# Optimization experiments

Measured on AMD Instinct MI355X. Metric: run time of the kernel, lower is better.

The kernel has to match this reference:

```python
import jax, jax.numpy as jnp
import numpy as np

EPS = 1e-5

def group_points(feat, idx):
    # feat: [B, C, N1], idx: [B, N2, K] -> [B, C, N2, K]
    return jax.vmap(lambda f, i: f[:, i])(feat, idx)

def conv_bn_relu(x, W, gamma, beta):
    # 1x1 conv2d (no bias) + training-mode BatchNorm2d + ReLU
    y = jnp.einsum('oc,bcnk->bonk', W, x)
    mean = y.mean(axis=(0, 2, 3), keepdims=True)
    var = y.var(axis=(0, 2, 3), keepdims=True)  # biased, as BN uses for normalization
    y = (y - mean) * jax.lax.rsqrt(var + EPS)
    y = y * gamma[None, :, None, None] + beta[None, :, None, None]
    return jax.nn.relu(y)

def setup_inputs() -> dict:
    key = jax.random.key(0)
    ks = jax.random.split(key, 12)
    B, N1, N2, K, C1 = 16, 4096, 1024, 32, 64
    mlp = [C1 + 3, 64, 64, 128]  # use_xyz adds 3 channels
    inp = {
        'in_xyz': jax.random.normal(ks[0], (B, 3, N1), jnp.float32),
        'out_xyz': jax.random.normal(ks[1], (B, 3, N2), jnp.float32),
        'in_feature': jax.random.normal(ks[2], (B, C1, N1), jnp.float32),
        'nbr_index': jax.random.randint(ks[3], (B, N2, K), 0, N1, jnp.int32),
    }
    for li in range(3):
        cin, cout = mlp[li], mlp[li + 1]
        inp[f'W{li}'] = jax.random.normal(ks[4 + li], (cout, cin), jnp.float32) * (1.0 / np.sqrt(cin))
        inp[f'g{li}'] = jnp.ones((cout,), jnp.float32)
        inp[f'b{li}'] = jnp.zeros((cout,), jnp.float32)
    return inp

def reference(in_xyz, out_xyz, in_feature, nbr_index,
              W0, g0, b0, W1, g1, b1, W2, g2, b2):
    # gather neighbor features: [B, C1, N2, K]
    nbr_feature = group_points(in_feature, nbr_index)
    # gather neighbor xyz, recenter on query points: [B, 3, N2, K]
    nbr_xyz = group_points(in_xyz, nbr_index) - out_xyz[:, :, :, None]
    x = jnp.concatenate([nbr_feature, nbr_xyz], axis=1)  # [B, C1+3, N2, K]
    x = conv_bn_relu(x, W0, g0, b0)
    x = conv_bn_relu(x, W1, g1, b1)
    x = conv_bn_relu(x, W2, g2, b2)
    return jnp.max(x, axis=3)  # [B, C2, N2]
```

## Files before the change

### kernel.cpp

```cpp
#include <hip/hip_runtime.h>
#include <cstdint>

typedef unsigned short u16;
typedef unsigned int   u32;
typedef __attribute__((ext_vector_type(8))) short  short8;
typedef __attribute__((ext_vector_type(4))) float  floatx4;

#define NPTS 524288

__device__ __forceinline__ float b2f(u16 h) { return __uint_as_float(((u32)h) << 16); }
__device__ __forceinline__ u16 f2b(float f) {
  u32 u = __float_as_uint(f);
  return (u16)((u + 0x7FFFu + ((u >> 16) & 1u)) >> 16);
}
__device__ __forceinline__ u32 pk_bf16(float lo, float hi) {
  return (u32)f2b(lo) | ((u32)f2b(hi) << 16);
}
__device__ __forceinline__ short8 ld_frag8(const u16* p) {
  union { uint4 q; short8 s; } x;
  x.q = *(const uint4*)p;
  return x.s;
}
__device__ __forceinline__ void bar_lds() {
  asm volatile("s_waitcnt lgkmcnt(0)\n\ts_barrier" ::: "memory");
}

__global__ __launch_bounds__(256) void prep_all(const float* __restrict__ inf,
                                                const float* __restrict__ ixyz,
                                                const float* __restrict__ oxyz,
                                                const int* __restrict__ nbr,
                                                const float* __restrict__ W0,
                                                const float* __restrict__ W1,
                                                const float* __restrict__ W2,
                                                u16* __restrict__ featT,
                                                uint2* __restrict__ dxyz,
                                                u16* __restrict__ Wb,
                                                u32* __restrict__ cnt,
                                                float* __restrict__ accz) {
  __shared__ float tile[32 * 33];
  const int bk = blockIdx.x, t = threadIdx.x;
  if (bk < 4096) {
    int b = bk >> 8, rem = bk & 255, cc = rem >> 7, nc = rem & 127;
    #pragma unroll
    for (int i = 0; i < 4; ++i) {
      int flat = t + i * 256;
      int cl = flat >> 5, nl = flat & 31;
      tile[cl * 33 + nl] = inf[(size_t)((b * 64) + cc * 32 + cl) * 4096 + nc * 32 + nl];
    }
    __syncthreads();
    #pragma unroll
    for (int i = 0; i < 4; ++i) {
      int flat = t + i * 256;
      int nl = flat >> 5, cl = flat & 31;
      featT[(size_t)((b << 12) + nc * 32 + nl) * 64 + cc * 32 + cl] = f2b(tile[cl * 33 + nl]);
    }
  } else if (bk < 6144) {
    int g = (bk - 4096) * 256 + t;
    int b = g >> 15, r = g & 32767, n2 = r >> 5;
    int id = nbr[g];
    const float* ix = ixyz + (size_t)b * 12288;
    const float* ox = oxyz + (size_t)b * 3072;
    float dx = ix[id]        - ox[n2];
    float dy = ix[4096 + id] - ox[1024 + n2];
    float dzv = ix[8192 + id] - ox[2048 + n2];
    dxyz[g] = make_uint2(pk_bf16(dx, dy), pk_bf16(dzv, 0.f));
  } else {
    int s = (bk - 6144) * 256 + t;
    u16 v = 0;
    if (s < 6656)       { int o = s / 104, c = s % 104; if (c < 67) v = f2b(W0[o * 67 + c]); }
    else if (s < 11264) { int q = s - 6656;  int o = q / 72, c = q % 72; if (c < 64) v = f2b(W1[o * 64 + c]); }
    else                { int q = s - 11264; int o = q / 72, c = q % 72; if (c < 64) v = f2b(W2[o * 64 + c]); }
    Wb[s] = v;
    if (bk == 6144) {
      if (t < 4) cnt[t] = 0u;
      accz[t] = 0.f;
      accz[256 + t] = 0.f;
    }
  }
}

template<int KSTEPS, int OCH, bool GATHER, bool MAXOUT>
__global__ __launch_bounds__(256, 4) void gemm_layer(
    const u16* __restrict__ xsrc, const uint2* __restrict__ dxyz,
    const int* __restrict__ nbr,
    const u16* __restrict__ Wb, const float* __restrict__ ssin,
    u16* __restrict__ yout, u32* __restrict__ gm,
    float* __restrict__ partial) {
  constexpr int PITCH = KSTEPS * 32 + 8;
  __shared__ __align__(16) u16 xs[2][64 * PITCH];
  __shared__ float red[512];
  __shared__ float ss[GATHER ? 4 : 128];

  const int t = threadIdx.x, blk = blockIdx.x;
  const int lane = t & 63, wv = t >> 6, lr = lane & 15, quad = lane >> 4;
  const int m = t >> 2, s4 = t & 3;
  const int P0 = blk * 256;
  const int b = blk >> 7;
  const int rg = wv >> 1, cg = wv & 1;

  short8 wf[4][KSTEPS];
  #pragma unroll
  for (int nt = 0; nt < 4; ++nt) {
    const int orow = (MAXOUT ? cg * 64 : 0) + nt * 16 + lr;
    const u16* wr = Wb + orow * PITCH + quad * 8;
    #pragma unroll
    for (int ks = 0; ks < KSTEPS; ++ks)
      wf[nt][ks] = ld_frag8(wr + ks * 32);
  }

  if constexpr (!GATHER) {
    if (t < 128) ss[t] = ssin[t];
  }
  if constexpr (GATHER) {
    #pragma unroll
    for (int bu = 0; bu < 2; ++bu) {
      if (s4 == 1) {
        u16* xr = xs[bu] + m * PITCH;
        #pragma unroll
        for (int j = 0; j < 9; ++j) *(uint2*)(xr + 68 + j * 4) = make_uint2(0u, 0u);
      }
    }
  }
  if constexpr (!GATHER) __syncthreads();

  int idx4[4];
  if constexpr (GATHER) {
    #pragma unroll
    for (int sub = 0; sub < 4; ++sub) idx4[sub] = nbr[P0 + sub * 64 + m];
  }

  uint4 f0, f1;
  uint2 dz = make_uint2(0u, 0u);

  auto issue = [&](int sub) {
    const int P = P0 + sub * 64 + m;
    if constexpr (GATHER) {
      const int id = idx4[sub];
      const u16* row = xsrc + ((size_t)((b << 12) + id)) * 64;
      f0 = *(const uint4*)(row + s4 * 16);
      f1 = *(const uint4*)(row + s4 * 16 + 8);
      if (s4 == 0) dz = dxyz[P];
    } else {
      const u16* row = xsrc + ((size_t)P << 6);
      f0 = *(const uint4*)(row + s4 * 16);
      f1 = *(const uint4*)(row + s4 * 16 + 8);
    }
  };

  auto commit = [&](int bu) {
    u16* xrow = xs[bu] + m * PITCH + s4 * 16;
    if constexpr (GATHER) {
      *(uint4*)(xrow + 0) = f0;
      *(uint4*)(xrow + 8) = f1;
      if (s4 == 0) *(uint2*)(xs[bu] + m * PITCH + 64) = dz;
    } else {
      u32 w[8] = { f0.x, f0.y, f0.z, f0.w, f1.x, f1.y, f1.z, f1.w };
      u32 o[8];
      #pragma unroll
      for (int i = 0; i < 8; ++i) {
        const int c = s4 * 16 + i * 2;
        float lo = fmaxf(b2f((u16)(w[i] & 0xffffu)) * ss[c]     + ss[64 + c],     0.f);
        float hi = fmaxf(b2f((u16)(w[i] >> 16))     * ss[c + 1] + ss[64 + c + 1], 0.f);
        o[i] = pk_bf16(lo, hi);
      }
      *(uint4*)(xrow + 0) = make_uint4(o[0], o[1], o[2], o[3]);
      *(uint4*)(xrow + 8) = make_uint4(o[4], o[5], o[6], o[7]);
    }
  };

  issue(0); commit(0);
  issue(1);
  __syncthreads();

  float s1[4] = {0.f, 0.f, 0.f, 0.f}, s2[4] = {0.f, 0.f, 0.f, 0.f};
  u32* yo = (u32*)yout;

  for (int sub = 0; sub < 4; ++sub) {
    const int cur = sub & 1;
    if (sub < 3) commit(cur ^ 1);
    if (sub < 2) issue(sub + 2);

    if constexpr (!MAXOUT) {
      const u16* ap = xs[cur] + (wv * 16 + lr) * PITCH + quad * 8;
      floatx4 acc[4];
      #pragma unroll
      for (int nt = 0; nt < 4; ++nt) acc[nt] = (floatx4){0.f, 0.f, 0.f, 0.f};
      #pragma unroll
      for (int ks = 0; ks < KSTEPS; ++ks) {
        short8 av = ld_frag8(ap + ks * 32);
        #pragma unroll
        for (int nt = 0; nt < 4; ++nt)
          acc[nt] = __builtin_amdgcn_mfma_f32_16x16x32_bf16(av, wf[nt][ks], acc[nt], 0, 0, 0);
      }
      const int R0 = P0 + sub * 64 + wv * 16 + quad * 4;
      #pragma unroll
      for (int nt = 0; nt < 4; ++nt) {
        #pragma unroll
        for (int r = 0; r < 4; ++r) {
          float v = acc[nt][r];
          s1[nt] += v; s2[nt] += v * v;
          float vo = __shfl_xor(v, 1);
          if ((lr & 1) == 0)
            yo[(size_t)(R0 + r) * 32 + nt * 8 + (lr >> 1)] = pk_bf16(v, vo);
        }
      }
    } else {
      short8 av[2][KSTEPS];
      #pragma unroll
      for (int h = 0; h < 2; ++h)
        #pragma unroll
        for (int ks = 0; ks < KSTEPS; ++ks)
          av[h][ks] = ld_frag8(xs[cur] + (rg * 32 + h * 16 + lr) * PITCH + quad * 8 + ks * 32);
      floatx4 acc[2][4];
      #pragma unroll
      for (int h = 0; h < 2; ++h)
        #pragma unroll
        for (int nt = 0; nt < 4; ++nt) acc[h][nt] = (floatx4){0.f, 0.f, 0.f, 0.f};
      #pragma unroll
      for (int ks = 0; ks < KSTEPS; ++ks)
        #pragma unroll
        for (int nt = 0; nt < 4; ++nt)
          #pragma unroll
          for (int h = 0; h < 2; ++h)
            acc[h][nt] = __builtin_amdgcn_mfma_f32_16x16x32_bf16(av[h][ks], wf[nt][ks], acc[h][nt], 0, 0, 0);
      float mx[4], mn[4];
      #pragma unroll
      for (int nt = 0; nt < 4; ++nt) {
        mx[nt] = -INFINITY; mn[nt] = INFINITY;
        #pragma unroll
        for (int h = 0; h < 2; ++h)
          #pragma unroll
          for (int r = 0; r < 4; ++r) {
            float v = acc[h][nt][r];
            s1[nt] += v; s2[nt] += v * v;
            mx[nt] = fmaxf(mx[nt], v); mn[nt] = fminf(mn[nt], v);
          }
        mx[nt] = fmaxf(mx[nt], __shfl_xor(mx[nt], 16));
        mx[nt] = fmaxf(mx[nt], __shfl_xor(mx[nt], 32));
        mn[nt] = fminf(mn[nt], __shfl_xor(mn[nt], 16));
        mn[nt] = fminf(mn[nt], __shfl_xor(mn[nt], 32));
      }
      if (lane < 16) {
        const int grp = blk * 8 + sub * 2 + rg;
        #pragma unroll
        for (int nt = 0; nt < 4; ++nt)
          gm[(size_t)grp * 128 + cg * 64 + nt * 16 + lr] = pk_bf16(mx[nt], mn[nt]);
      }
    }
    if (sub < 3) bar_lds();
  }

  #pragma unroll
  for (int nt = 0; nt < 4; ++nt) {
    s1[nt] += __shfl_xor(s1[nt], 16); s1[nt] += __shfl_xor(s1[nt], 32);
    s2[nt] += __shfl_xor(s2[nt], 16); s2[nt] += __shfl_xor(s2[nt], 32);
  }
  if (lane < 16) {
    #pragma unroll
    for (int nt = 0; nt < 4; ++nt) {
      red[wv * 64 + nt * 16 + lr] = s1[nt];
      red[256 + wv * 64 + nt * 16 + lr] = s2[nt];
    }
  }
  __syncthreads();
  if constexpr (!MAXOUT) {
    if (t < 64) {
      partial[(size_t)blk * 128 + t] = red[t] + red[64 + t] + red[128 + t] + red[192 + t];
    } else if (t < 128) {
      int c = t - 64;
      partial[(size_t)blk * 128 + t] = red[256 + c] + red[320 + c] + red[384 + c] + red[448 + c];
    }
  } else {
    if (t < 128) {
      int half = t >> 6, i = t & 63;
      partial[(size_t)blk * 256 + t] = red[half * 64 + i] + red[(half + 2) * 64 + i];
    } else {
      int c = t - 128, half = c >> 6, i = c & 63;
      partial[(size_t)blk * 256 + t] = red[256 + half * 64 + i] + red[256 + (half + 2) * 64 + i];
    }
  }
}

__global__ __launch_bounds__(256) void bn_stats(const float* __restrict__ partial,
                                                float* __restrict__ accv,
                                                const float* __restrict__ gam,
                                                const float* __restrict__ bet,
                                                float* __restrict__ ssout,
                                                u32* __restrict__ counter, int och) {
  __shared__ float l[256];
  __shared__ u32 rank;
  const int cols = 2 * och, t = threadIdx.x;
  if (t < cols) {
    const size_t r0 = (size_t)blockIdx.x * 32;
    float s = 0.f;
    for (int r = 0; r < 32; ++r) s += partial[(r0 + r) * cols + t];
    atomicAdd(&accv[t], s);
  }
  __threadfence();
  __syncthreads();
  if (t == 0) rank = atomicAdd(counter, 1u);
  __syncthreads();
  if (rank != 63) return;
  __threadfence();
  if (t < cols) l[t] = accv[t];
  __syncthreads();
  if (t < och) {
    const float invN = 1.f / (float)NPTS;
    float mean = l[t] * invN;
    float var  = fmaxf(l[och + t] * invN - mean * mean, 0.f);
    float scale = gam[t] * rsqrtf(var + 1e-5f);
    ssout[t] = scale;
    ssout[och + t] = bet[t] - mean * scale;
  }
}

__global__ __launch_bounds__(256) void final_out(const u32* __restrict__ gm,
                                                 const float* __restrict__ ss2,
                                                 float* __restrict__ out) {
  __shared__ float tile[64 * 33];
  int blk = blockIdx.x;
  int b = blk >> 6, rem = blk & 63, cc = rem >> 4, nn = rem & 15;
  int t = threadIdx.x;
  #pragma unroll
  for (int i = 0; i < 8; ++i) {
    int flat = t + i * 256;
    int n2l = flat >> 5, cl = flat & 31;
    int c = cc * 32 + cl;
    size_t idx = (size_t)((b << 10) + nn * 64 + n2l) * 128 + c;
    u32 p = gm[idx];
    float mx = b2f((u16)(p & 0xffffu)), mn = b2f((u16)(p >> 16));
    float scv = ss2[c], shv = ss2[128 + c];
    float v = (scv >= 0.f) ? mx : mn;
    tile[n2l * 33 + cl] = fmaxf(scv * v + shv, 0.f);
  }
  __syncthreads();
  #pragma unroll
  for (int i = 0; i < 8; ++i) {
    int flat = t + i * 256;
    int cl = flat >> 6, n2l = flat & 63;
    out[(size_t)((b * 128) + cc * 32 + cl) * 1024 + nn * 64 + n2l] = tile[n2l * 33 + cl];
  }
}

extern "C" void kernel_launch(void* const* d_in, const int* in_sizes, int n_in,
                              void* d_out, int out_size, void* d_ws, size_t ws_size,
                              hipStream_t stream) {
  const float* in_xyz  = (const float*)d_in[0];
  const float* out_xyz = (const float*)d_in[1];
  const float* in_feat = (const float*)d_in[2];
  const int*   nbr     = (const int*)d_in[3];
  const float* W0 = (const float*)d_in[4];
  const float* g0 = (const float*)d_in[5];
  const float* b0 = (const float*)d_in[6];
  const float* W1 = (const float*)d_in[7];
  const float* g1 = (const float*)d_in[8];
  const float* b1 = (const float*)d_in[9];
  const float* W2 = (const float*)d_in[10];
  const float* g2 = (const float*)d_in[11];
  const float* b2 = (const float*)d_in[12];
  float* out = (float*)d_out;

  char* ws = (char*)d_ws;
  float*  ssbuf = (float*)(ws + 0);
  u32*    cnt   = (u32*)(ws + 3072);
  float*  accv  = (float*)(ws + 3584);
  u16*    Wb    = (u16*)(ws + 8192);
  u16*    featT = (u16*)(ws + 262144);
  uint2*  dxyz  = (uint2*)(ws + 8650752);
  u16*    y0    = (u16*)(ws + 13631488);
  u16*    y1    = (u16*)(ws + 80740352);
  float*  p0    = (float*)(ws + 80740352);
  float*  p1    = (float*)(ws + 262144);
  u32*    gm    = (u32*)(ws + 13631488);
  float*  p2    = (float*)(ws + 13631488 + 8388608);

  hipLaunchKernelGGL(prep_all, dim3(6224), dim3(256), 0, stream,
                     in_feat, in_xyz, out_xyz, nbr, W0, W1, W2, featT, dxyz, Wb, cnt, accv);

  hipLaunchKernelGGL((gemm_layer<3, 64, true, false>), dim3(2048), dim3(256), 0, stream,
                     featT, dxyz, nbr, Wb, nullptr, y0, nullptr, p0);
  hipLaunchKernelGGL(bn_stats, dim3(64), dim3(256), 0, stream,
                     p0, accv, g0, b0, ssbuf, cnt, 64);

  hipLaunchKernelGGL((gemm_layer<2, 64, false, false>), dim3(2048), dim3(256), 0, stream,
                     y0, nullptr, nullptr, Wb + 6656, ssbuf, y1, nullptr, p1);
  hipLaunchKernelGGL(bn_stats, dim3(64), dim3(256), 0, stream,
                     p1, accv + 128, g1, b1, ssbuf + 256, cnt + 1, 64);

  hipLaunchKernelGGL((gemm_layer<2, 128, false, true>), dim3(2048), dim3(256), 0, stream,
                     y1, nullptr, nullptr, Wb + 11264, ssbuf + 256, nullptr, gm, p2);
  hipLaunchKernelGGL(bn_stats, dim3(64), dim3(256), 0, stream,
                     p2, accv + 256, g2, b2, ssbuf + 512, cnt + 2, 128);

  hipLaunchKernelGGL(final_out, dim3(1024), dim3(256), 0, stream, gm, ssbuf + 512, out);
}
```

Before: 214.2 us.

## Apply first conv before gathering and add xyz contribution per neighbor

Computes the first-layer 1x1 conv on the 64 feature channels once per input point (before the neighbor gather), then gathers those projected features and adds the 3-channel xyz term with scalar FMAs while accumulating BN statistics. This removes the separate feature transpose and dxyz precompute passes and cuts the layer-0 matrix work by the neighbor fan-out. It adds an extra intermediate bf16 rounding of the projected features and a new uncoalesced-ish strided fp32 read in the pre-GEMM kernel.

Result: no change. 213.9 us (-0.1%).

```diff
diff --git a/kernel.cpp b/kernel.cpp
--- a/kernel.cpp
+++ b/kernel.cpp
@@ -25,147 +25,203 @@
   asm volatile("s_waitcnt lgkmcnt(0)\n\ts_barrier" ::: "memory");
 }
 
-__global__ __launch_bounds__(256) void prep_all(const float* __restrict__ inf,
-                                                const float* __restrict__ ixyz,
-                                                const float* __restrict__ oxyz,
-                                                const int* __restrict__ nbr,
-                                                const float* __restrict__ W0,
+__global__ __launch_bounds__(256) void prep_all(const float* __restrict__ W0,
                                                 const float* __restrict__ W1,
                                                 const float* __restrict__ W2,
-                                                u16* __restrict__ featT,
-                                                uint2* __restrict__ dxyz,
                                                 u16* __restrict__ Wb,
                                                 u32* __restrict__ cnt,
                                                 float* __restrict__ accz) {
-  __shared__ float tile[32 * 33];
   const int bk = blockIdx.x, t = threadIdx.x;
-  if (bk < 4096) {
-    int b = bk >> 8, rem = bk & 255, cc = rem >> 7, nc = rem & 127;
-    #pragma unroll
-    for (int i = 0; i < 4; ++i) {
-      int flat = t + i * 256;
-      int cl = flat >> 5, nl = flat & 31;
-      tile[cl * 33 + nl] = inf[(size_t)((b * 64) + cc * 32 + cl) * 4096 + nc * 32 + nl];
-    }
-    __syncthreads();
-    #pragma unroll
-    for (int i = 0; i < 4; ++i) {
-      int flat = t + i * 256;
-      int nl = flat >> 5, cl = flat & 31;
-      featT[(size_t)((b << 12) + nc * 32 + nl) * 64 + cc * 32 + cl] = f2b(tile[cl * 33 + nl]);
-    }
-  } else if (bk < 6144) {
-    int g = (bk - 4096) * 256 + t;
-    int b = g >> 15, r = g & 32767, n2 = r >> 5;
-    int id = nbr[g];
-    const float* ix = ixyz + (size_t)b * 12288;
-    const float* ox = oxyz + (size_t)b * 3072;
-    float dx = ix[id]        - ox[n2];
-    float dy = ix[4096 + id] - ox[1024 + n2];
-    float dzv = ix[8192 + id] - ox[2048 + n2];
-    dxyz[g] = make_uint2(pk_bf16(dx, dy), pk_bf16(dzv, 0.f));
-  } else {
-    int s = (bk - 6144) * 256 + t;
-    u16 v = 0;
-    if (s < 6656)       { int o = s / 104, c = s % 104; if (c < 67) v = f2b(W0[o * 67 + c]); }
-    else if (s < 11264) { int q = s - 6656;  int o = q / 72, c = q % 72; if (c < 64) v = f2b(W1[o * 64 + c]); }
-    else                { int q = s - 11264; int o = q / 72, c = q % 72; if (c < 64) v = f2b(W2[o * 64 + c]); }
-    Wb[s] = v;
-    if (bk == 6144) {
-      if (t < 4) cnt[t] = 0u;
-      accz[t] = 0.f;
-      accz[256 + t] = 0.f;
-    }
-  }
-}
-
-template<int KSTEPS, int OCH, bool GATHER, bool MAXOUT>
+  int s = bk * 256 + t;
+  u16 v = 0;
+  if (s < 4608)      { int o = s / 72, c = s % 72; if (c < 64) v = f2b(W0[o * 67 + c]); }
+  else if (s < 9216) { int q = s - 4608; int o = q / 72, c = q % 72; if (c < 64) v = f2b(W1[o * 64 + c]); }
+  else               { int q = s - 9216; int o = q / 72, c = q % 72; if (c < 64) v = f2b(W2[o * 64 + c]); }
+  Wb[s] = v;
+  if (bk == 0) {
+    if (t < 4) cnt[t] = 0u;
+    accz[t] = 0.f;
+    accz[256 + t] = 0.f;
+  }
+}
+
+__global__ __launch_bounds__(256) void zgemm(const float* __restrict__ inf,
+                                             const u16* __restrict__ Wb,
+                                             u16* __restrict__ z) {
+  const int t = threadIdx.x, blk = blockIdx.x;
+  const int lane = t & 63, wv = t >> 6, lr = lane & 15, quad = lane >> 4;
+  const int b = blk >> 6, n0 = (blk & 63) * 64;
+
+  short8 wf[4][2];
+  #pragma unroll
+  for (int nt = 0; nt < 4; ++nt) {
+    const u16* wr = Wb + (nt * 16 + lr) * 72 + quad * 8;
+    #pragma unroll
+    for (int ks = 0; ks < 2; ++ks) wf[nt][ks] = ld_frag8(wr + ks * 32);
+  }
+
+  const float* fb = inf + (size_t)b * 262144 + (n0 + wv * 16 + lr);
+  short8 av[2];
+  #pragma unroll
+  for (int ks = 0; ks < 2; ++ks) {
+    union { u32 u[4]; short8 s; } a;
+    #pragma unroll
+    for (int j = 0; j < 4; ++j) {
+      int c0 = ks * 32 + quad * 8 + 2 * j;
+      a.u[j] = pk_bf16(fb[(size_t)c0 * 4096], fb[(size_t)(c0 + 1) * 4096]);
+    }
+    av[ks] = a.s;
+  }
+
+  floatx4 acc[4];
+  #pragma unroll
+  for (int nt = 0; nt < 4; ++nt) acc[nt] = (floatx4){0.f, 0.f, 0.f, 0.f};
+  #pragma unroll
+  for (int ks = 0; ks < 2; ++ks)
+    #pragma unroll
+    for (int nt = 0; nt < 4; ++nt)
+      acc[nt] = __builtin_amdgcn_mfma_f32_16x16x32_bf16(av[ks], wf[nt][ks], acc[nt], 0, 0, 0);
+
+  u32* zo = (u32*)z;
+  const int R0 = b * 4096 + n0 + wv * 16 + quad * 4;
+  #pragma unroll
+  for (int nt = 0; nt < 4; ++nt) {
+    #pragma unroll
+    for (int r = 0; r < 4; ++r) {
+      float v = acc[nt][r];
+      float vo = __shfl_xor(v, 1);
+      if ((lr & 1) == 0)
+        zo[(size_t)(R0 + r) * 32 + nt * 8 + (lr >> 1)] = pk_bf16(v, vo);
+    }
+  }
+}
+
+__global__ __launch_bounds__(256) void gather_add(const u16* __restrict__ z,
+                                                  const float* __restrict__ ixyz,
+                                                  const float* __restrict__ oxyz,
+                                                  const int* __restrict__ nbr,
+                                                  const float* __restrict__ W0,
+                                                  u16* __restrict__ y0,
+                                                  float* __restrict__ partial) {
+  __shared__ float wx[64], wy[64], wz[64];
+  __shared__ float red[512];
+  const int t = threadIdx.x, blk = blockIdx.x;
+  if (t < 64) {
+    wx[t] = W0[t * 67 + 64];
+    wy[t] = W0[t * 67 + 65];
+    wz[t] = W0[t * 67 + 66];
+  }
+  __syncthreads();
+  const int s4 = t & 3;
+  const int b = blk >> 7;
+  const float* ix = ixyz + (size_t)b * 12288;
+  const float* ox = oxyz + (size_t)b * 3072;
+
+  float s1[16], s2[16];
+  #pragma unroll
+  for (int i = 0; i < 16; ++i) { s1[i] = 0.f; s2[i] = 0.f; }
+
+  int idx[4], n2v[4];
+  #pragma unroll
+  for (int u = 0; u < 4; ++u) {
+    int row = blk * 256 + u * 64 + (t >> 2);
+    idx[u] = nbr[row];
+    n2v[u] = (row >> 5) & 1023;
+  }
+
+  #pragma unroll
+  for (int u = 0; u < 4; ++u) {
+    const int id = idx[u];
+    const u16* zr = z + ((size_t)(b << 12) + id) * 64 + s4 * 16;
+    uint4 a0 = *(const uint4*)zr;
+    uint4 a1 = *(const uint4*)(zr + 8);
+    float dx = ix[id]        - ox[n2v[u]];
+    float dy = ix[4096 + id] - ox[1024 + n2v[u]];
+    float dzv = ix[8192 + id] - ox[2048 + n2v[u]];
+    u32 w[8] = { a0.x, a0.y, a0.z, a0.w, a1.x, a1.y, a1.z, a1.w };
+    u32 o[8];
+    #pragma unroll
+    for (int i = 0; i < 8; ++i) {
+      int c = s4 * 16 + 2 * i;
+      float lo = b2f((u16)(w[i] & 0xffffu)) + wx[c] * dx + wy[c] * dy + wz[c] * dzv;
+      float hi = b2f((u16)(w[i] >> 16)) + wx[c + 1] * dx + wy[c + 1] * dy + wz[c + 1] * dzv;
+      s1[2 * i] += lo;     s2[2 * i] += lo * lo;
+      s1[2 * i + 1] += hi; s2[2 * i + 1] += hi * hi;
+      o[i] = pk_bf16(lo, hi);
+    }
+    int row = blk * 256 + u * 64 + (t >> 2);
+    u16* yrow = y0 + (size_t)row * 64 + s4 * 16;
+    *(uint4*)yrow = make_uint4(o[0], o[1], o[2], o[3]);
+    *(uint4*)(yrow + 8) = make_uint4(o[4], o[5], o[6], o[7]);
+  }
+
+  #pragma unroll
+  for (int i = 0; i < 16; ++i) {
+    s1[i] += __shfl_xor(s1[i], 4);  s2[i] += __shfl_xor(s2[i], 4);
+    s1[i] += __shfl_xor(s1[i], 8);  s2[i] += __shfl_xor(s2[i], 8);
+    s1[i] += __shfl_xor(s1[i], 16); s2[i] += __shfl_xor(s2[i], 16);
+    s1[i] += __shfl_xor(s1[i], 32); s2[i] += __shfl_xor(s2[i], 32);
+  }
+  const int wv = t >> 6, lane = t & 63;
+  if (lane < 4) {
+    #pragma unroll
+    for (int i = 0; i < 16; ++i) {
+      red[wv * 128 + lane * 16 + i] = s1[i];
+      red[wv * 128 + 64 + lane * 16 + i] = s2[i];
+    }
+  }
+  __syncthreads();
+  if (t < 128)
+    partial[(size_t)blk * 128 + t] = red[t] + red[128 + t] + red[256 + t] + red[384 + t];
+}
+
+template<int OCH, bool MAXOUT>
 __global__ __launch_bounds__(256, 4) void gemm_layer(
-    const u16* __restrict__ xsrc, const uint2* __restrict__ dxyz,
-    const int* __restrict__ nbr,
-    const u16* __restrict__ Wb, const float* __restrict__ ssin,
-    u16* __restrict__ yout, u32* __restrict__ gm,
-    float* __restrict__ partial) {
-  constexpr int PITCH = KSTEPS * 32 + 8;
+    const u16* __restrict__ xsrc, const u16* __restrict__ Wb,
+    const float* __restrict__ ssin, u16* __restrict__ yout,
+    u32* __restrict__ gm, float* __restrict__ partial) {
+  constexpr int PITCH = 72;
   __shared__ __align__(16) u16 xs[2][64 * PITCH];
   __shared__ float red[512];
-  __shared__ float ss[GATHER ? 4 : 128];
+  __shared__ float ss[128];
 
   const int t = threadIdx.x, blk = blockIdx.x;
   const int lane = t & 63, wv = t >> 6, lr = lane & 15, quad = lane >> 4;
   const int m = t >> 2, s4 = t & 3;
   const int P0 = blk * 256;
-  const int b = blk >> 7;
   const int rg = wv >> 1, cg = wv & 1;
 
-  short8 wf[4][KSTEPS];
+  short8 wf[4][2];
   #pragma unroll
   for (int nt = 0; nt < 4; ++nt) {
     const int orow = (MAXOUT ? cg * 64 : 0) + nt * 16 + lr;
     const u16* wr = Wb + orow * PITCH + quad * 8;
     #pragma unroll
-    for (int ks = 0; ks < KSTEPS; ++ks)
-      wf[nt][ks] = ld_frag8(wr + ks * 32);
-  }
-
-  if constexpr (!GATHER) {
-    if (t < 128) ss[t] = ssin[t];
-  }
-  if constexpr (GATHER) {
-    #pragma unroll
-    for (int bu = 0; bu < 2; ++bu) {
-      if (s4 == 1) {
-        u16* xr = xs[bu] + m * PITCH;
-        #pragma unroll
-        for (int j = 0; j < 9; ++j) *(uint2*)(xr + 68 + j * 4) = make_uint2(0u, 0u);
-      }
-    }
-  }
-  if constexpr (!GATHER) __syncthreads();
-
-  int idx4[4];
-  if constexpr (GATHER) {
-    #pragma unroll
-    for (int sub = 0; sub < 4; ++sub) idx4[sub] = nbr[P0 + sub * 64 + m];
-  }
+    for (int ks = 0; ks < 2; ++ks) wf[nt][ks] = ld_frag8(wr + ks * 32);
+  }
+
+  if (t < 128) ss[t] = ssin[t];
+  __syncthreads();
 
   uint4 f0, f1;
-  uint2 dz = make_uint2(0u, 0u);
-
   auto issue = [&](int sub) {
-    const int P = P0 + sub * 64 + m;
-    if constexpr (GATHER) {
-      const int id = idx4[sub];
-      const u16* row = xsrc + ((size_t)((b << 12) + id)) * 64;
-      f0 = *(const uint4*)(row + s4 * 16);
-      f1 = *(const uint4*)(row + s4 * 16 + 8);
-      if (s4 == 0) dz = dxyz[P];
-    } else {
-      const u16* row = xsrc + ((size_t)P << 6);
-      f0 = *(const uint4*)(row + s4 * 16);
-      f1 = *(const uint4*)(row + s4 * 16 + 8);
-    }
+    const u16* row = xsrc + ((size_t)(P0 + sub * 64 + m) << 6);
+    f0 = *(const uint4*)(row + s4 * 16);
+    f1 = *(const uint4*)(row + s4 * 16 + 8);
   };
-
   auto commit = [&](int bu) {
     u16* xrow = xs[bu] + m * PITCH + s4 * 16;
-    if constexpr (GATHER) {
-      *(uint4*)(xrow + 0) = f0;
-      *(uint4*)(xrow + 8) = f1;
-      if (s4 == 0) *(uint2*)(xs[bu] + m * PITCH + 64) = dz;
-    } else {
-      u32 w[8] = { f0.x, f0.y, f0.z, f0.w, f1.x, f1.y, f1.z, f1.w };
-      u32 o[8];
-      #pragma unroll
-      for (int i = 0; i < 8; ++i) {
-        const int c = s4 * 16 + i * 2;
-        float lo = fmaxf(b2f((u16)(w[i] & 0xffffu)) * ss[c]     + ss[64 + c],     0.f);
-        float hi = fmaxf(b2f((u16)(w[i] >> 16))     * ss[c + 1] + ss[64 + c + 1], 0.f);
-        o[i] = pk_bf16(lo, hi);
-      }
-      *(uint4*)(xrow + 0) = make_uint4(o[0], o[1], o[2], o[3]);
-      *(uint4*)(xrow + 8) = make_uint4(o[4], o[5], o[6], o[7]);
-    }
+    u32 w[8] = { f0.x, f0.y, f0.z, f0.w, f1.x, f1.y, f1.z, f1.w };
+    u32 o[8];
+    #pragma unroll
+    for (int i = 0; i < 8; ++i) {
+      const int c = s4 * 16 + i * 2;
+      float lo = fmaxf(b2f((u16)(w[i] & 0xffffu)) * ss[c]     + ss[64 + c],     0.f);
+      float hi = fmaxf(b2f((u16)(w[i] >> 16))     * ss[c + 1] + ss[64 + c + 1], 0.f);
+      o[i] = pk_bf16(lo, hi);
+    }
+    *(uint4*)(xrow + 0) = make_uint4(o[0], o[1], o[2], o[3]);
+    *(uint4*)(xrow + 8) = make_uint4(o[4], o[5], o[6], o[7]);
   };
 
   issue(0); commit(0);
@@ -186,7 +242,7 @@
       #pragma unroll
       for (int nt = 0; nt < 4; ++nt) acc[nt] = (floatx4){0.f, 0.f, 0.f, 0.f};
       #pragma unroll
-      for (int ks = 0; ks < KSTEPS; ++ks) {
+      for (int ks = 0; ks < 2; ++ks) {
         short8 av = ld_frag8(ap + ks * 32);
         #pragma unroll
         for (int nt = 0; nt < 4; ++nt)
@@ -205,11 +261,11 @@
         }
       }
     } else {
-      short8 av[2][KSTEPS];
+      short8 av[2][2];
       #pragma unroll
       for (int h = 0; h < 2; ++h)
         #pragma unroll
-        for (int ks = 0; ks < KSTEPS; ++ks)
+        for (int ks = 0; ks < 2; ++ks)
           av[h][ks] = ld_frag8(xs[cur] + (rg * 32 + h * 16 + lr) * PITCH + quad * 8 + ks * 32);
       floatx4 acc[2][4];
       #pragma unroll
@@ -217,7 +273,7 @@
         #pragma unroll
         for (int nt = 0; nt < 4; ++nt) acc[h][nt] = (floatx4){0.f, 0.f, 0.f, 0.f};
       #pragma unroll
-      for (int ks = 0; ks < KSTEPS; ++ks)
+      for (int ks = 0; ks < 2; ++ks)
         #pragma unroll
         for (int nt = 0; nt < 4; ++nt)
           #pragma unroll
@@ -365,30 +421,29 @@
   u32*    cnt   = (u32*)(ws + 3072);
   float*  accv  = (float*)(ws + 3584);
   u16*    Wb    = (u16*)(ws + 8192);
-  u16*    featT = (u16*)(ws + 262144);
-  uint2*  dxyz  = (uint2*)(ws + 8650752);
-  u16*    y0    = (u16*)(ws + 13631488);
-  u16*    y1    = (u16*)(ws + 80740352);
-  float*  p0    = (float*)(ws + 80740352);
+  u16*    z     = (u16*)(ws + 262144);
+  u16*    y0    = (u16*)(ws + 8650752);
+  u16*    y1    = (u16*)(ws + 75759616);
+  float*  p0    = (float*)(ws + 75759616);
   float*  p1    = (float*)(ws + 262144);
-  u32*    gm    = (u32*)(ws + 13631488);
-  float*  p2    = (float*)(ws + 13631488 + 8388608);
-
-  hipLaunchKernelGGL(prep_all, dim3(6224), dim3(256), 0, stream,
-                     in_feat, in_xyz, out_xyz, nbr, W0, W1, W2, featT, dxyz, Wb, cnt, accv);
-
-  hipLaunchKernelGGL((gemm_layer<3, 64, true, false>), dim3(2048), dim3(256), 0, stream,
-                     featT, dxyz, nbr, Wb, nullptr, y0, nullptr, p0);
+  u32*    gm    = (u32*)(ws + 8650752);
+  float*  p2    = (float*)(ws + 8650752 + 8388608);
+
+  hipLaunchKernelGGL(prep_all, dim3(72), dim3(256), 0, stream, W0, W1, W2, Wb, cnt, accv);
+
+  hipLaunchKernelGGL(zgemm, dim3(1024), dim3(256), 0, stream, in_feat, Wb, z);
+  hipLaunchKernelGGL(gather_add, dim3(2048), dim3(256), 0, stream,
+                     z, in_xyz, out_xyz, nbr, W0, y0, p0);
   hipLaunchKernelGGL(bn_stats, dim3(64), dim3(256), 0, stream,
                      p0, accv, g0, b0, ssbuf, cnt, 64);
 
-  hipLaunchKernelGGL((gemm_layer<2, 64, false, false>), dim3(2048), dim3(256), 0, stream,
-                     y0, nullptr, nullptr, Wb + 6656, ssbuf, y1, nullptr, p1);
+  hipLaunchKernelGGL((gemm_layer<64, false>), dim3(2048), dim3(256), 0, stream,
+                     y0, Wb + 4608, ssbuf, y1, nullptr, p1);
   hipLaunchKernelGGL(bn_stats, dim3(64), dim3(256), 0, stream,
                      p1, accv + 128, g1, b1, ssbuf + 256, cnt + 1, 64);
 
-  hipLaunchKernelGGL((gemm_layer<2, 128, false, true>), dim3(2048), dim3(256), 0, stream,
-                     y1, nullptr, nullptr, Wb + 11264, ssbuf + 256, nullptr, gm, p2);
+  hipLaunchKernelGGL((gemm_layer<128, true>), dim3(2048), dim3(256), 0, stream,
+                     y1, Wb + 9216, ssbuf + 256, nullptr, gm, p2);
   hipLaunchKernelGGL(bn_stats, dim3(64), dim3(256), 0, stream,
                      p2, accv + 256, g2, b2, ssbuf + 512, cnt + 2, 128);
 
```
